# Optimization experiments

Hardware: AMD Instinct MI355X
Metric: run time of the kernel (lower is better)

Reference implementation:

```python
import jax, jax.numpy as jnp
import numpy as np

G = 8      # num_codebooks
D = 64     # codebook_dim
V = 1024   # codebook_size
BETA = 1.0


def setup_inputs() -> dict:
    key = jax.random.key(0)
    k1, k2, k3 = jax.random.split(key, 3)
    inputs = jax.random.normal(k1, (8, 2048, G * D), dtype=jnp.float32)
    paddings = jax.random.randint(k2, (8, 2048), 0, 2, dtype=jnp.int32)
    codebook = jax.random.normal(k3, (V, G, D), dtype=jnp.float32)
    return {"inputs": inputs, "paddings": paddings, "codebook": codebook}


def reference(inputs, paddings, codebook):
    B, T, _ = inputs.shape
    x = inputs.reshape(B, T, G, D)

    # Per-group L2 nearest neighbor: dist[b,t,g,v] = ||x - c||^2
    # ||x||^2 is constant over v, drop it for the argmin.
    dots = jnp.einsum("btgd,vgd->btgv", x, codebook)          # [B,T,G,V]
    c_sq = jnp.sum(codebook * codebook, axis=-1)                # [V,G]
    dists = c_sq.T[None, None] - 2.0 * dots                     # [B,T,G,V]
    ids = jnp.argmin(dists, axis=-1)                            # [B,T,G]

    # Gather selected codes per group.
    quantized = codebook[ids, jnp.arange(G)[None, None, :]]     # [B,T,G,D]

    mask = (1.0 - paddings.astype(jnp.float32))[:, :, None, None]  # [B,T,1,1]
    denom = mask.sum()
    xd = jax.lax.stop_gradient(x)
    qd = jax.lax.stop_gradient(quantized)
    kmeans_loss = jnp.sum((quantized - xd) ** 2 * mask) / denom
    commitment_loss = jnp.sum((x - qd) ** 2 * mask) / denom
    total_loss = kmeans_loss + BETA * commitment_loss

    # Straight-through estimator, masked.
    quantized_st = (x + jax.lax.stop_gradient(quantized - x)) * mask
    quantized_st = quantized_st.reshape(B, T, G * D)

    ids = jnp.where(mask[:, :, :, 0] == 0.0, -1, ids)           # [B,T,G]
    return ids, quantized_st, kmeans_loss, commitment_loss, total_loss
```

## Files before the change

### kernel.cpp

```cpp
#include <hip/hip_runtime.h>
#include <cfloat>
#include <stdint.h>

#define G_ 8
#define D_ 64
#define V_ 1024
#define BT_ 16384
#define TPB_ 512
#define PREPB_ 256
#define NSLOT_ 128
#define TOKS_ 128
#define NC_ 128
#define NCHUNK_ (V_ / NC_)

typedef unsigned long long u64;
typedef uint32_t u32;
typedef _Float16 h8 __attribute__((ext_vector_type(8)));
typedef _Float16 h4 __attribute__((ext_vector_type(4)));
typedef float f32x4 __attribute__((ext_vector_type(4)));

typedef __attribute__((address_space(3))) uint32_t lds_u32;
typedef __attribute__((address_space(1))) uint32_t glb_u32;

#define GL2LDS(gsrc, ldst) \
    __builtin_amdgcn_global_load_lds((glb_u32*)(gsrc), (lds_u32*)(ldst), 16, 0, 0)


__global__ void prep_csq(const float* __restrict__ cb, const int* __restrict__ pad,
                         float* __restrict__ csqT,
                         int* __restrict__ cnt, int* __restrict__ list,
                         float* __restrict__ out_ids, float* __restrict__ out_q,
                         _Float16* __restrict__ cbH, _Float16* __restrict__ cbL) {
    const int tid = threadIdx.x;
    const int idx = blockIdx.x * PREPB_ + tid;

    if (idx < V_ * G_) {
        const float4* r = (const float4*)(cb + (size_t)idx * D_);
        _Float16* hp = cbH + (size_t)idx * 64;
        _Float16* lp = cbL + (size_t)idx * 64;
        float s = 0.f;
#pragma unroll
        for (int i = 0; i < D_ / 4; ++i) {
            float4 c = r[i];
            s += c.x * c.x + c.y * c.y + c.z * c.z + c.w * c.w;
            float xs[4] = {c.x, c.y, c.z, c.w};
            h4 hv, lv;
#pragma unroll
            for (int e = 0; e < 4; ++e) {
                _Float16 hh = (_Float16)xs[e];
                hv[e] = hh;
                lv[e] = (_Float16)((xs[e] - (float)hh) * 4096.f);
            }
            *(h4*)(hp + i * 4) = hv;
            *(h4*)(lp + i * 4) = lv;
        }
        csqT[(idx & (G_ - 1)) * V_ + (idx >> 3)] = s;
    }

    __shared__ int s_cnt[8];
    __shared__ int s_base, s_npl;
    __shared__ int s_plist[PREPB_];
    const int lane = tid & 63, w = tid >> 6;
    const bool active = (pad[idx] == 0);
    u64 bal = __ballot(active);
    int na  = __popcll(bal);
    if (lane == 0) { s_cnt[w] = na; s_cnt[4 + w] = 64 - na; }
    __syncthreads();
    if (tid == 0) {
        int ta = s_cnt[0] + s_cnt[1] + s_cnt[2] + s_cnt[3];
        s_base = atomicAdd(cnt, ta);
        s_npl  = PREPB_ - ta;
    }
    __syncthreads();
    int pre_a = 0, pre_p = 0;
    for (int i = 0; i < w; ++i) { pre_a += s_cnt[i]; pre_p += s_cnt[4 + i]; }
    const u64 mb = ((u64)1 << lane) - 1;
    if (active) list[s_base + pre_a + __popcll(bal & mb)] = idx;
    else        s_plist[pre_p + __popcll(~bal & mb)] = idx;
    __syncthreads();

    const int npl = s_npl;
    for (int i = w; i < npl; i += 4) {
        int tok = s_plist[i];
        float4 z = make_float4(0.f, 0.f, 0.f, 0.f);
        float4* q = (float4*)(out_q + (size_t)tok * (G_ * D_)) + lane * 2;
        q[0] = z;
        q[1] = z;
        if (lane < G_) out_ids[(size_t)tok * G_ + lane] = -1.0f;
    }
}

__global__ __launch_bounds__(TPB_, 4) void vq_scan(
    const float* __restrict__ inp,
    const float* __restrict__ cb,
    const float* __restrict__ csqT,
    const int* __restrict__ cnt,
    const int* __restrict__ list,
    const _Float16* __restrict__ cbH,
    const _Float16* __restrict__ cbL,
    float* __restrict__ out_ids,
    float* __restrict__ out_q,
    float* __restrict__ part) {

    __shared__ __align__(16) unsigned char BH[2][NC_ * 128];
    __shared__ __align__(16) unsigned char BL[2][NC_ * 128];
    __shared__ float csq_s[V_];
    __shared__ u64 merge_s[2][TOKS_];

    const int nact = cnt[0];
    const int tile = blockIdx.x;
    if (tile * TOKS_ >= nact) return;
    const int g    = blockIdx.y;
    const int tid  = threadIdx.x;
    const int lane = tid & 63;
    const int w    = tid >> 6;
    const int mh   = w >> 1;
    const int nh   = w & 1;
    const int r16  = lane & 15;
    const int kq   = lane >> 4;

    const size_t soff = (size_t)(w * 8 + (lane >> 3)) * 1024
                      + (size_t)g * 128
                      + (size_t)(((lane & 7) ^ (lane >> 3)) * 16);
    const unsigned char* sH = (const unsigned char*)cbH + soff;
    const unsigned char* sL = (const unsigned char*)cbL + soff;
    const int ldsb = w * 1024;

    GL2LDS(sH,         &BH[0][ldsb]);
    GL2LDS(sH + 65536, &BH[0][ldsb + 8192]);
    GL2LDS(sL,         &BL[0][ldsb]);
    GL2LDS(sL + 65536, &BL[0][ldsb + 8192]);

    csq_s[tid]       = csqT[g * V_ + tid];
    csq_s[tid + 512] = csqT[g * V_ + tid + 512];

    h8 AH[2][2], AL[2][2];
#pragma unroll
    for (int rf = 0; rf < 2; ++rf) {
        int p = tile * TOKS_ + mh * 32 + rf * 16 + r16;
        int tok = list[p < nact ? p : 0];
        const float* xr = inp + (size_t)tok * (G_ * D_) + g * D_;
#pragma unroll
        for (int kf = 0; kf < 2; ++kf) {
            const float4* xp = (const float4*)(xr + kf * 32 + kq * 8);
            float4 a = xp[0], b = xp[1];
            float xs[8] = {a.x, a.y, a.z, a.w, b.x, b.y, b.z, b.w};
#pragma unroll
            for (int e = 0; e < 8; ++e) {
                _Float16 hh = (_Float16)xs[e];
                AH[rf][kf][e] = hh;
                AL[rf][kf][e] = (_Float16)((xs[e] - (float)hh) * 4096.f);
            }
        }
    }

    float beste[8];
    int   bestid[8];
#pragma unroll
    for (int s = 0; s < 8; ++s) { beste[s] = -FLT_MAX / 2; bestid[s] = 0; }

    __syncthreads();

    const u32 o0 = (u32)((((nh * 64 + r16) * 128 + kq * 16))
                         ^ ((u32)(r16 & 7) << 4));

    for (int c = 0; c < NCHUNK_; ++c) {
        const int cur = c & 1;
        const unsigned char* BHc = &BH[cur][0];
        const unsigned char* BLc = &BL[cur][0];

        if (c < NCHUNK_ - 1) {
            unsigned char* dH = &BH[cur ^ 1][ldsb];
            unsigned char* dL = &BL[cur ^ 1][ldsb];
            const unsigned char* nH = sH + (size_t)(c + 1) * 131072;
            const unsigned char* nL = sL + (size_t)(c + 1) * 131072;
            GL2LDS(nH,         dH);
            GL2LDS(nH + 65536, dH + 8192);
            GL2LDS(nL,         dL);
            GL2LDS(nL + 65536, dL + 8192);
        }

#pragma unroll 1
        for (int cf = 0; cf < 4; ++cf) {
            const u32 ob = o0 + (u32)(cf * 2048);
            const h8 bh0 = *(const h8*)(BHc + ob);
            const h8 bh1 = *(const h8*)(BHc + (ob ^ 64));
            const h8 bl0 = *(const h8*)(BLc + ob);
            const h8 bl1 = *(const h8*)(BLc + (ob ^ 64));
            const int vcol = c * NC_ + nh * 64 + cf * 16 + r16;
            const float ai = -0.5f * csq_s[vcol];
#pragma unroll
            for (int rf = 0; rf < 2; ++rf) {
                f32x4 a  = {ai, ai, ai, ai};
                f32x4 ac = {0.f, 0.f, 0.f, 0.f};
                a  = __builtin_amdgcn_mfma_f32_16x16x32_f16(AH[rf][0], bh0, a,  0, 0, 0);
                a  = __builtin_amdgcn_mfma_f32_16x16x32_f16(AH[rf][1], bh1, a,  0, 0, 0);
                ac = __builtin_amdgcn_mfma_f32_16x16x32_f16(AH[rf][0], bl0, ac, 0, 0, 0);
                ac = __builtin_amdgcn_mfma_f32_16x16x32_f16(AH[rf][1], bl1, ac, 0, 0, 0);
                ac = __builtin_amdgcn_mfma_f32_16x16x32_f16(AL[rf][0], bh0, ac, 0, 0, 0);
                ac = __builtin_amdgcn_mfma_f32_16x16x32_f16(AL[rf][1], bh1, ac, 0, 0, 0);
#pragma unroll
                for (int q = 0; q < 4; ++q) {
                    float e = fmaf(0x1.0p-12f, ac[q], a[q]);
                    int s = rf * 4 + q;
                    if (e > beste[s]) { beste[s] = e; bestid[s] = vcol; }
                }
            }
        }
        __syncthreads();
    }

#pragma unroll
    for (int s = 0; s < 8; ++s) {
        float d = -2.f * beste[s];
        u32 u = __float_as_uint(d);
        u = u ^ ((u >> 31) ? 0xFFFFFFFFu : 0x80000000u);
        u64 pk = ((u64)u << 32) | (u32)bestid[s];
#pragma unroll
        for (int off = 1; off <= 8; off <<= 1) {
            u64 o = __shfl_xor(pk, off, 64);
            pk = (o < pk) ? o : pk;
        }
        if (r16 == 0) {
            int row = mh * 32 + (s >> 2) * 16 + kq * 4 + (s & 3);
            merge_s[nh][row] = pk;
        }
    }
    __syncthreads();

    float l = 0.f;
    {
        int tl = tid >> 2, qv = tid & 3;
        int p  = tile * TOKS_ + tl;
        if (p < nact) {
            int tok = list[p];
            u64 qa = merge_s[0][tl], qb = merge_s[1][tl];
            u64 qm = (qb < qa) ? qb : qa;
            int id  = (int)(qm & 0xFFFFFFFFull);
            const float4* cr = (const float4*)(cb + ((size_t)id * G_ + g) * D_) + qv * 4;
            const float4* xr = (const float4*)(inp + (size_t)tok * (G_ * D_) + g * D_) + qv * 4;
            float4* qo = (float4*)(out_q + (size_t)tok * (G_ * D_) + g * D_) + qv * 4;
#pragma unroll
            for (int k = 0; k < 4; ++k) {
                float4 cc = cr[k], xx = xr[k];
                float dx = cc.x - xx.x, dy = cc.y - xx.y;
                float dz = cc.z - xx.z, dw = cc.w - xx.w;
                l += dx * dx + dy * dy + dz * dz + dw * dw;
                qo[k] = cc;
            }
            if (qv == 0) out_ids[(size_t)tok * G_ + g] = (float)id;
        }
    }
#pragma unroll
    for (int off = 32; off > 0; off >>= 1) l += __shfl_down(l, off, 64);
    if (lane == 0) {
        int slot = ((blockIdx.y * gridDim.x + blockIdx.x) * 8 + w) & (NSLOT_ - 1);
        atomicAdd(&part[slot], l);
    }
}

__global__ void finalize_kernel(const float* __restrict__ part,
                                const int* __restrict__ cnt,
                                float* __restrict__ out_losses) {
    int lane = threadIdx.x;
    float l = part[lane] + part[lane + 64];
#pragma unroll
    for (int off = 32; off > 0; off >>= 1) l += __shfl_down(l, off, 64);
    if (lane == 0) {
        float k = l / (float)cnt[0];
        out_losses[0] = k;
        out_losses[1] = k;
        out_losses[2] = 2.f * k;
    }
}

extern "C" void kernel_launch(void* const* d_in, const int* in_sizes, int n_in,
                              void* d_out, int out_size, void* d_ws, size_t ws_size,
                              hipStream_t stream) {
    const float* inp = (const float*)d_in[0];
    const int*   pad = (const int*)d_in[1];
    const float* cb  = (const float*)d_in[2];

    float* out   = (float*)d_out;
    float* o_ids = out;
    float* o_q   = out + (size_t)BT_ * G_;
    float* o_ls  = o_q + (size_t)BT_ * G_ * D_;

    float*     part = (float*)d_ws;
    int*       cnt  = (int*)((char*)d_ws + 512);
    float*     csqT = (float*)((char*)d_ws + 1024);
    int*       list = (int*)((char*)d_ws + 33792);
    _Float16*  cbH  = (_Float16*)((char*)d_ws + 131072);
    _Float16*  cbL  = (_Float16*)((char*)d_ws + 131072 + 1048576);

    hipMemsetAsync(d_ws, 0, 1024, stream);

    prep_csq<<<dim3(BT_ / PREPB_), dim3(PREPB_), 0, stream>>>(
        cb, pad, csqT, cnt, list, o_ids, o_q, cbH, cbL);

    dim3 grid(BT_ / TOKS_, G_);
    vq_scan<<<grid, dim3(TPB_), 0, stream>>>(
        inp, cb, csqT, cnt, list, cbH, cbL, o_ids, o_q, part);

    finalize_kernel<<<1, dim3(64), 0, stream>>>(part, cnt, o_ls);
}
```

Measured before the change: 138.7 us.

## Load codebook fragments directly from global memory and split V across waves

Removes the double-buffered LDS staging of the fp16 hi/lo codebook (global_load_lds plus per-chunk barriers). Each of four waves now scans its own quarter of the codebook for all 64 tokens of the tile, reading B fragments straight from global/L2, and the four partial argmins are merged in shared memory. Block size drops to 256 threads with 64 tokens per tile, and each wave holds four A row fragments. The point is to drop barrier and LDS overhead and raise A reuse per B load, at the price of more register pressure and uncoalesced, L2-dependent codebook reads.

After: 158.2 us. 14.1% more time.

```diff
diff --git a/kernel.cpp b/kernel.cpp
--- a/kernel.cpp
+++ b/kernel.cpp
@@ -6,24 +6,17 @@
 #define D_ 64
 #define V_ 1024
 #define BT_ 16384
-#define TPB_ 512
+#define TPB_ 256
 #define PREPB_ 256
 #define NSLOT_ 128
-#define TOKS_ 128
-#define NC_ 128
-#define NCHUNK_ (V_ / NC_)
+#define TOKS_ 64
+#define NCF_ 16
 
 typedef unsigned long long u64;
 typedef uint32_t u32;
 typedef _Float16 h8 __attribute__((ext_vector_type(8)));
 typedef _Float16 h4 __attribute__((ext_vector_type(4)));
 typedef float f32x4 __attribute__((ext_vector_type(4)));
-
-typedef __attribute__((address_space(3))) uint32_t lds_u32;
-typedef __attribute__((address_space(1))) uint32_t glb_u32;
-
-#define GL2LDS(gsrc, ldst) \
-    __builtin_amdgcn_global_load_lds((glb_u32*)(gsrc), (lds_u32*)(ldst), 16, 0, 0)
 
 
 __global__ void prep_csq(const float* __restrict__ cb, const int* __restrict__ pad,
@@ -90,7 +83,7 @@
     }
 }
 
-__global__ __launch_bounds__(TPB_, 4) void vq_scan(
+__global__ __launch_bounds__(TPB_, 3) void vq_scan(
     const float* __restrict__ inp,
     const float* __restrict__ cb,
     const float* __restrict__ csqT,
@@ -102,10 +95,7 @@
     float* __restrict__ out_q,
     float* __restrict__ part) {
 
-    __shared__ __align__(16) unsigned char BH[2][NC_ * 128];
-    __shared__ __align__(16) unsigned char BL[2][NC_ * 128];
-    __shared__ float csq_s[V_];
-    __shared__ u64 merge_s[2][TOKS_];
+    __shared__ u64 merge_s[4][TOKS_];
 
     const int nact = cnt[0];
     const int tile = blockIdx.x;
@@ -114,30 +104,13 @@
     const int tid  = threadIdx.x;
     const int lane = tid & 63;
     const int w    = tid >> 6;
-    const int mh   = w >> 1;
-    const int nh   = w & 1;
     const int r16  = lane & 15;
     const int kq   = lane >> 4;
 
-    const size_t soff = (size_t)(w * 8 + (lane >> 3)) * 1024
-                      + (size_t)g * 128
-                      + (size_t)(((lane & 7) ^ (lane >> 3)) * 16);
-    const unsigned char* sH = (const unsigned char*)cbH + soff;
-    const unsigned char* sL = (const unsigned char*)cbL + soff;
-    const int ldsb = w * 1024;
-
-    GL2LDS(sH,         &BH[0][ldsb]);
-    GL2LDS(sH + 65536, &BH[0][ldsb + 8192]);
-    GL2LDS(sL,         &BL[0][ldsb]);
-    GL2LDS(sL + 65536, &BL[0][ldsb + 8192]);
-
-    csq_s[tid]       = csqT[g * V_ + tid];
-    csq_s[tid + 512] = csqT[g * V_ + tid + 512];
-
-    h8 AH[2][2], AL[2][2];
-#pragma unroll
-    for (int rf = 0; rf < 2; ++rf) {
-        int p = tile * TOKS_ + mh * 32 + rf * 16 + r16;
+    h8 AH[4][2], AL[4][2];
+#pragma unroll
+    for (int rf = 0; rf < 4; ++rf) {
+        int p = tile * TOKS_ + rf * 16 + r16;
         int tok = list[p < nact ? p : 0];
         const float* xr = inp + (size_t)tok * (G_ * D_) + g * D_;
 #pragma unroll
@@ -154,64 +127,43 @@
         }
     }
 
-    float beste[8];
-    int   bestid[8];
-#pragma unroll
-    for (int s = 0; s < 8; ++s) { beste[s] = -FLT_MAX / 2; bestid[s] = 0; }
-
-    __syncthreads();
-
-    const u32 o0 = (u32)((((nh * 64 + r16) * 128 + kq * 16))
-                         ^ ((u32)(r16 & 7) << 4));
-
-    for (int c = 0; c < NCHUNK_; ++c) {
-        const int cur = c & 1;
-        const unsigned char* BHc = &BH[cur][0];
-        const unsigned char* BLc = &BL[cur][0];
-
-        if (c < NCHUNK_ - 1) {
-            unsigned char* dH = &BH[cur ^ 1][ldsb];
-            unsigned char* dL = &BL[cur ^ 1][ldsb];
-            const unsigned char* nH = sH + (size_t)(c + 1) * 131072;
-            const unsigned char* nL = sL + (size_t)(c + 1) * 131072;
-            GL2LDS(nH,         dH);
-            GL2LDS(nH + 65536, dH + 8192);
-            GL2LDS(nL,         dL);
-            GL2LDS(nL + 65536, dL + 8192);
-        }
-
-#pragma unroll 1
-        for (int cf = 0; cf < 4; ++cf) {
-            const u32 ob = o0 + (u32)(cf * 2048);
-            const h8 bh0 = *(const h8*)(BHc + ob);
-            const h8 bh1 = *(const h8*)(BHc + (ob ^ 64));
-            const h8 bl0 = *(const h8*)(BLc + ob);
-            const h8 bl1 = *(const h8*)(BLc + (ob ^ 64));
-            const int vcol = c * NC_ + nh * 64 + cf * 16 + r16;
-            const float ai = -0.5f * csq_s[vcol];
-#pragma unroll
-            for (int rf = 0; rf < 2; ++rf) {
-                f32x4 a  = {ai, ai, ai, ai};
-                f32x4 ac = {0.f, 0.f, 0.f, 0.f};
-                a  = __builtin_amdgcn_mfma_f32_16x16x32_f16(AH[rf][0], bh0, a,  0, 0, 0);
-                a  = __builtin_amdgcn_mfma_f32_16x16x32_f16(AH[rf][1], bh1, a,  0, 0, 0);
-                ac = __builtin_amdgcn_mfma_f32_16x16x32_f16(AH[rf][0], bl0, ac, 0, 0, 0);
-                ac = __builtin_amdgcn_mfma_f32_16x16x32_f16(AH[rf][1], bl1, ac, 0, 0, 0);
-                ac = __builtin_amdgcn_mfma_f32_16x16x32_f16(AL[rf][0], bh0, ac, 0, 0, 0);
-                ac = __builtin_amdgcn_mfma_f32_16x16x32_f16(AL[rf][1], bh1, ac, 0, 0, 0);
-#pragma unroll
-                for (int q = 0; q < 4; ++q) {
-                    float e = fmaf(0x1.0p-12f, ac[q], a[q]);
-                    int s = rf * 4 + q;
-                    if (e > beste[s]) { beste[s] = e; bestid[s] = vcol; }
-                }
-            }
-        }
-        __syncthreads();
-    }
-
-#pragma unroll
-    for (int s = 0; s < 8; ++s) {
+    float beste[16];
+    int   bestid[16];
+#pragma unroll
+    for (int s = 0; s < 16; ++s) { beste[s] = -FLT_MAX / 2; bestid[s] = 0; }
+
+    const int v0 = w * 256;
+#pragma unroll 2
+    for (int c = 0; c < NCF_; ++c) {
+        const int vc = v0 + c * 16 + r16;
+        const _Float16* bh = cbH + ((size_t)vc * G_ + g) * D_ + kq * 8;
+        const _Float16* bl = cbL + ((size_t)vc * G_ + g) * D_ + kq * 8;
+        const h8 bh0 = *(const h8*)bh;
+        const h8 bh1 = *(const h8*)(bh + 32);
+        const h8 bl0 = *(const h8*)bl;
+        const h8 bl1 = *(const h8*)(bl + 32);
+        const float ai = -0.5f * csqT[g * V_ + vc];
+#pragma unroll
+        for (int rf = 0; rf < 4; ++rf) {
+            f32x4 a  = {ai, ai, ai, ai};
+            f32x4 ac = {0.f, 0.f, 0.f, 0.f};
+            a  = __builtin_amdgcn_mfma_f32_16x16x32_f16(AH[rf][0], bh0, a,  0, 0, 0);
+            a  = __builtin_amdgcn_mfma_f32_16x16x32_f16(AH[rf][1], bh1, a,  0, 0, 0);
+            ac = __builtin_amdgcn_mfma_f32_16x16x32_f16(AH[rf][0], bl0, ac, 0, 0, 0);
+            ac = __builtin_amdgcn_mfma_f32_16x16x32_f16(AH[rf][1], bl1, ac, 0, 0, 0);
+            ac = __builtin_amdgcn_mfma_f32_16x16x32_f16(AL[rf][0], bh0, ac, 0, 0, 0);
+            ac = __builtin_amdgcn_mfma_f32_16x16x32_f16(AL[rf][1], bh1, ac, 0, 0, 0);
+#pragma unroll
+            for (int q = 0; q < 4; ++q) {
+                float e = fmaf(0x1.0p-12f, ac[q], a[q]);
+                int s = rf * 4 + q;
+                if (e > beste[s]) { beste[s] = e; bestid[s] = vc; }
+            }
+        }
+    }
+
+#pragma unroll
+    for (int s = 0; s < 16; ++s) {
         float d = -2.f * beste[s];
         u32 u = __float_as_uint(d);
         u = u ^ ((u >> 31) ? 0xFFFFFFFFu : 0x80000000u);
@@ -222,8 +174,8 @@
             pk = (o < pk) ? o : pk;
         }
         if (r16 == 0) {
-            int row = mh * 32 + (s >> 2) * 16 + kq * 4 + (s & 3);
-            merge_s[nh][row] = pk;
+            int row = (s >> 2) * 16 + kq * 4 + (s & 3);
+            merge_s[w][row] = pk;
         }
     }
     __syncthreads();
@@ -234,7 +186,10 @@
         int p  = tile * TOKS_ + tl;
         if (p < nact) {
             int tok = list[p];
-            u64 qa = merge_s[0][tl], qb = merge_s[1][tl];
+            u64 q0 = merge_s[0][tl], q1 = merge_s[1][tl];
+            u64 q2 = merge_s[2][tl], q3 = merge_s[3][tl];
+            u64 qa = (q1 < q0) ? q1 : q0;
+            u64 qb = (q3 < q2) ? q3 : q2;
             u64 qm = (qb < qa) ? qb : qa;
             int id  = (int)(qm & 0xFFFFFFFFull);
             const float4* cr = (const float4*)(cb + ((size_t)id * G_ + g) * D_) + qv * 4;
@@ -254,7 +209,7 @@
 #pragma unroll
     for (int off = 32; off > 0; off >>= 1) l += __shfl_down(l, off, 64);
     if (lane == 0) {
-        int slot = ((blockIdx.y * gridDim.x + blockIdx.x) * 8 + w) & (NSLOT_ - 1);
+        int slot = ((blockIdx.y * gridDim.x + blockIdx.x) * 4 + w) & (NSLOT_ - 1);
         atomicAdd(&part[slot], l);
     }
 }
```

## Halve block size, deepen codebook LDS pipeline to 4 buffers with raw barriers

Applied to the files above, without the earlier changes.

The scan kernel now runs with 256 threads per block, each wave owning 64 tokens instead of 32. Codebook chunks shrink to 64 codes and go through a 4-deep LDS ring with three chunks prefetched ahead. Each iteration uses one manual vmcnt wait plus s_barrier in place of __syncthreads after compute. The goal is more B-fragment reuse per LDS read and better hiding of global-to-LDS latency. In exchange it doubles per-thread accumulator and A-fragment registers, lowers the occupancy target, and relies on hand-counted vmcnt values being correct.

After: 134.6 us. 1.03x faster.

```diff
diff --git a/kernel.cpp b/kernel.cpp
--- a/kernel.cpp
+++ b/kernel.cpp
@@ -6,11 +6,12 @@
 #define D_ 64
 #define V_ 1024
 #define BT_ 16384
-#define TPB_ 512
+#define TPB_ 256
 #define PREPB_ 256
 #define NSLOT_ 128
 #define TOKS_ 128
-#define NC_ 128
+#define NC_ 64
+#define NB_ 4
 #define NCHUNK_ (V_ / NC_)
 
 typedef unsigned long long u64;
@@ -90,7 +91,7 @@
     }
 }
 
-__global__ __launch_bounds__(TPB_, 4) void vq_scan(
+__global__ __launch_bounds__(TPB_, 2) void vq_scan(
     const float* __restrict__ inp,
     const float* __restrict__ cb,
     const float* __restrict__ csqT,
@@ -102,8 +103,8 @@
     float* __restrict__ out_q,
     float* __restrict__ part) {
 
-    __shared__ __align__(16) unsigned char BH[2][NC_ * 128];
-    __shared__ __align__(16) unsigned char BL[2][NC_ * 128];
+    __shared__ __align__(16) unsigned char BH[NB_][NC_ * 128];
+    __shared__ __align__(16) unsigned char BL[NB_][NC_ * 128];
     __shared__ float csq_s[V_];
     __shared__ u64 merge_s[2][TOKS_];
 
@@ -119,25 +120,10 @@
     const int r16  = lane & 15;
     const int kq   = lane >> 4;
 
-    const size_t soff = (size_t)(w * 8 + (lane >> 3)) * 1024
-                      + (size_t)g * 128
-                      + (size_t)(((lane & 7) ^ (lane >> 3)) * 16);
-    const unsigned char* sH = (const unsigned char*)cbH + soff;
-    const unsigned char* sL = (const unsigned char*)cbL + soff;
-    const int ldsb = w * 1024;
-
-    GL2LDS(sH,         &BH[0][ldsb]);
-    GL2LDS(sH + 65536, &BH[0][ldsb + 8192]);
-    GL2LDS(sL,         &BL[0][ldsb]);
-    GL2LDS(sL + 65536, &BL[0][ldsb + 8192]);
-
-    csq_s[tid]       = csqT[g * V_ + tid];
-    csq_s[tid + 512] = csqT[g * V_ + tid + 512];
-
-    h8 AH[2][2], AL[2][2];
-#pragma unroll
-    for (int rf = 0; rf < 2; ++rf) {
-        int p = tile * TOKS_ + mh * 32 + rf * 16 + r16;
+    h8 AH[4][2], AL[4][2];
+#pragma unroll
+    for (int rf = 0; rf < 4; ++rf) {
+        int p = tile * TOKS_ + mh * 64 + rf * 16 + r16;
         int tok = list[p < nact ? p : 0];
         const float* xr = inp + (size_t)tok * (G_ * D_) + g * D_;
 #pragma unroll
@@ -154,43 +140,69 @@
         }
     }
 
-    float beste[8];
-    int   bestid[8];
-#pragma unroll
-    for (int s = 0; s < 8; ++s) { beste[s] = -FLT_MAX / 2; bestid[s] = 0; }
-
-    __syncthreads();
-
-    const u32 o0 = (u32)((((nh * 64 + r16) * 128 + kq * 16))
+    const size_t soff = (size_t)(w * 16 + (lane >> 3)) * 1024
+                      + (size_t)g * 128
+                      + (size_t)(((lane & 7) ^ (lane >> 3)) * 16);
+    const unsigned char* sH = (const unsigned char*)cbH + soff;
+    const unsigned char* sL = (const unsigned char*)cbL + soff;
+    const int ldsb = w * 2048;
+
+#pragma unroll
+    for (int c0 = 0; c0 < 3; ++c0) {
+        const size_t adv = (size_t)c0 * 65536;
+        GL2LDS(sH + adv,        &BH[c0][ldsb]);
+        GL2LDS(sH + adv + 8192, &BH[c0][ldsb + 1024]);
+        GL2LDS(sL + adv,        &BL[c0][ldsb]);
+        GL2LDS(sL + adv + 8192, &BL[c0][ldsb + 1024]);
+    }
+
+    csq_s[tid]       = csqT[g * V_ + tid];
+    csq_s[tid + 256] = csqT[g * V_ + tid + 256];
+    csq_s[tid + 512] = csqT[g * V_ + tid + 512];
+    csq_s[tid + 768] = csqT[g * V_ + tid + 768];
+
+    float beste[16];
+    int   bestid[16];
+#pragma unroll
+    for (int s = 0; s < 16; ++s) { beste[s] = -FLT_MAX / 2; bestid[s] = 0; }
+
+    asm volatile("s_waitcnt lgkmcnt(0)" ::: "memory");
+
+    const u32 o0 = (u32)((((nh * 32 + r16) * 128 + kq * 16))
                          ^ ((u32)(r16 & 7) << 4));
 
+#pragma unroll 1
     for (int c = 0; c < NCHUNK_; ++c) {
-        const int cur = c & 1;
-        const unsigned char* BHc = &BH[cur][0];
-        const unsigned char* BLc = &BL[cur][0];
-
-        if (c < NCHUNK_ - 1) {
-            unsigned char* dH = &BH[cur ^ 1][ldsb];
-            unsigned char* dL = &BL[cur ^ 1][ldsb];
-            const unsigned char* nH = sH + (size_t)(c + 1) * 131072;
-            const unsigned char* nL = sL + (size_t)(c + 1) * 131072;
-            GL2LDS(nH,         dH);
-            GL2LDS(nH + 65536, dH + 8192);
-            GL2LDS(nL,         dL);
-            GL2LDS(nL + 65536, dL + 8192);
-        }
-
-#pragma unroll 1
-        for (int cf = 0; cf < 4; ++cf) {
+        if (c < NCHUNK_ - 2)
+            asm volatile("s_waitcnt vmcnt(8)\n\ts_barrier" ::: "memory");
+        else if (c == NCHUNK_ - 2)
+            asm volatile("s_waitcnt vmcnt(4)\n\ts_barrier" ::: "memory");
+        else
+            asm volatile("s_waitcnt vmcnt(0)\n\ts_barrier" ::: "memory");
+        __builtin_amdgcn_sched_barrier(0);
+
+        if (c + 3 < NCHUNK_) {
+            const int b = (c + 3) & (NB_ - 1);
+            const size_t adv = (size_t)(c + 3) * 65536;
+            GL2LDS(sH + adv,        &BH[b][ldsb]);
+            GL2LDS(sH + adv + 8192, &BH[b][ldsb + 1024]);
+            GL2LDS(sL + adv,        &BL[b][ldsb]);
+            GL2LDS(sL + adv + 8192, &BL[b][ldsb + 1024]);
+        }
+
+        const unsigned char* BHc = &BH[c & (NB_ - 1)][0];
+        const unsigned char* BLc = &BL[c & (NB_ - 1)][0];
+#pragma unroll
+        for (int cf = 0; cf < 2; ++cf) {
             const u32 ob = o0 + (u32)(cf * 2048);
             const h8 bh0 = *(const h8*)(BHc + ob);
             const h8 bh1 = *(const h8*)(BHc + (ob ^ 64));
             const h8 bl0 = *(const h8*)(BLc + ob);
             const h8 bl1 = *(const h8*)(BLc + (ob ^ 64));
-            const int vcol = c * NC_ + nh * 64 + cf * 16 + r16;
+            const int vcol = c * NC_ + nh * 32 + cf * 16 + r16;
             const float ai = -0.5f * csq_s[vcol];
 #pragma unroll
-            for (int rf = 0; rf < 2; ++rf) {
+            for (int rf = 0; rf < 4; ++rf) {
                 f32x4 a  = {ai, ai, ai, ai};
                 f32x4 ac = {0.f, 0.f, 0.f, 0.f};
                 a  = __builtin_amdgcn_mfma_f32_16x16x32_f16(AH[rf][0], bh0, a,  0, 0, 0);
@@ -207,11 +219,10 @@
                 }
             }
         }
-        __syncthreads();
-    }
-
-#pragma unroll
-    for (int s = 0; s < 8; ++s) {
+    }
+
+#pragma unroll
+    for (int s = 0; s < 16; ++s) {
         float d = -2.f * beste[s];
         u32 u = __float_as_uint(d);
         u = u ^ ((u >> 31) ? 0xFFFFFFFFu : 0x80000000u);
@@ -222,7 +233,7 @@
             pk = (o < pk) ? o : pk;
         }
         if (r16 == 0) {
-            int row = mh * 32 + (s >> 2) * 16 + kq * 4 + (s & 3);
+            int row = mh * 64 + (s >> 2) * 16 + kq * 4 + (s & 3);
             merge_s[nh][row] = pk;
         }
     }
@@ -230,18 +241,18 @@
 
     float l = 0.f;
     {
-        int tl = tid >> 2, qv = tid & 3;
+        int tl = tid >> 1, qv = tid & 1;
         int p  = tile * TOKS_ + tl;
         if (p < nact) {
             int tok = list[p];
             u64 qa = merge_s[0][tl], qb = merge_s[1][tl];
             u64 qm = (qb < qa) ? qb : qa;
             int id  = (int)(qm & 0xFFFFFFFFull);
-            const float4* cr = (const float4*)(cb + ((size_t)id * G_ + g) * D_) + qv * 4;
-            const float4* xr = (const float4*)(inp + (size_t)tok * (G_ * D_) + g * D_) + qv * 4;
-            float4* qo = (float4*)(out_q + (size_t)tok * (G_ * D_) + g * D_) + qv * 4;
-#pragma unroll
-            for (int k = 0; k < 4; ++k) {
+            const float4* cr = (const float4*)(cb + ((size_t)id * G_ + g) * D_) + qv * 8;
+            const float4* xr = (const float4*)(inp + (size_t)tok * (G_ * D_) + g * D_) + qv * 8;
+            float4* qo = (float4*)(out_q + (size_t)tok * (G_ * D_) + g * D_) + qv * 8;
+#pragma unroll
+            for (int k = 0; k < 8; ++k) {
                 float4 cc = cr[k], xx = xr[k];
                 float dx = cc.x - xx.x, dy = cc.y - xx.y;
                 float dz = cc.z - xx.z, dw = cc.w - xx.w;
@@ -254,7 +265,7 @@
 #pragma unroll
     for (int off = 32; off > 0; off >>= 1) l += __shfl_down(l, off, 64);
     if (lane == 0) {
-        int slot = ((blockIdx.y * gridDim.x + blockIdx.x) * 8 + w) & (NSLOT_ - 1);
+        int slot = ((blockIdx.y * gridDim.x + blockIdx.x) * 4 + w) & (NSLOT_ - 1);
         atomicAdd(&part[slot], l);
     }
 }
```

## Halve block and chunk size, restructure codebook double-buffer with single barrier

Applied to the files above, without the earlier changes.

Block size drops from 512 to 256 threads, with 64 tokens per tile and 64-code chunks, so there are more, smaller blocks and less LDS per block. Codebook prefetch now starts after the A fragments are built. The main loop is restructured to one vmcnt wait plus barrier at the top of each chunk, which replaces the trailing __syncthreads, and the inner loop is fully unrolled. The intent is better occupancy and latency hiding, at the cost of more chunk iterations, more barriers overall and more repeated codebook loads across tiles.

Result: no change. 137.7 us (-0.7%).

```diff
diff --git a/kernel.cpp b/kernel.cpp
--- a/kernel.cpp
+++ b/kernel.cpp
@@ -6,11 +6,12 @@
 #define D_ 64
 #define V_ 1024
 #define BT_ 16384
-#define TPB_ 512
+#define TPB_ 256
 #define PREPB_ 256
 #define NSLOT_ 128
-#define TOKS_ 128
-#define NC_ 128
+#define TOKS_ 64
+#define NC_ 64
+#define NB_ 2
 #define NCHUNK_ (V_ / NC_)
 
 typedef unsigned long long u64;
@@ -102,8 +103,8 @@
     float* __restrict__ out_q,
     float* __restrict__ part) {
 
-    __shared__ __align__(16) unsigned char BH[2][NC_ * 128];
-    __shared__ __align__(16) unsigned char BL[2][NC_ * 128];
+    __shared__ __align__(16) unsigned char BH[NB_][NC_ * 128];
+    __shared__ __align__(16) unsigned char BL[NB_][NC_ * 128];
     __shared__ float csq_s[V_];
     __shared__ u64 merge_s[2][TOKS_];
 
@@ -119,21 +120,6 @@
     const int r16  = lane & 15;
     const int kq   = lane >> 4;
 
-    const size_t soff = (size_t)(w * 8 + (lane >> 3)) * 1024
-                      + (size_t)g * 128
-                      + (size_t)(((lane & 7) ^ (lane >> 3)) * 16);
-    const unsigned char* sH = (const unsigned char*)cbH + soff;
-    const unsigned char* sL = (const unsigned char*)cbL + soff;
-    const int ldsb = w * 1024;
-
-    GL2LDS(sH,         &BH[0][ldsb]);
-    GL2LDS(sH + 65536, &BH[0][ldsb + 8192]);
-    GL2LDS(sL,         &BL[0][ldsb]);
-    GL2LDS(sL + 65536, &BL[0][ldsb + 8192]);
-
-    csq_s[tid]       = csqT[g * V_ + tid];
-    csq_s[tid + 512] = csqT[g * V_ + tid + 512];
-
     h8 AH[2][2], AL[2][2];
 #pragma unroll
     for (int rf = 0; rf < 2; ++rf) {
@@ -154,40 +140,57 @@
         }
     }
 
+    const size_t soff = (size_t)(w * 16 + (lane >> 3)) * 1024
+                      + (size_t)g * 128
+                      + (size_t)(((lane & 7) ^ (lane >> 3)) * 16);
+    const unsigned char* sH = (const unsigned char*)cbH + soff;
+    const unsigned char* sL = (const unsigned char*)cbL + soff;
+    const int ldsb = w * 2048;
+
+    GL2LDS(sH,        &BH[0][ldsb]);
+    GL2LDS(sH + 8192, &BH[0][ldsb + 1024]);
+    GL2LDS(sL,        &BL[0][ldsb]);
+    GL2LDS(sL + 8192, &BL[0][ldsb + 1024]);
+
+    csq_s[tid]       = csqT[g * V_ + tid];
+    csq_s[tid + 256] = csqT[g * V_ + tid + 256];
+    csq_s[tid + 512] = csqT[g * V_ + tid + 512];
+    csq_s[tid + 768] = csqT[g * V_ + tid + 768];
+
     float beste[8];
     int   bestid[8];
 #pragma unroll
     for (int s = 0; s < 8; ++s) { beste[s] = -FLT_MAX / 2; bestid[s] = 0; }
 
-    __syncthreads();
-
-    const u32 o0 = (u32)((((nh * 64 + r16) * 128 + kq * 16))
+    asm volatile("s_waitcnt lgkmcnt(0)" ::: "memory");
+
+    const u32 o0 = (u32)((((nh * 32 + r16) * 128 + kq * 16))
                          ^ ((u32)(r16 & 7) << 4));
 
+#pragma unroll 1
     for (int c = 0; c < NCHUNK_; ++c) {
-        const int cur = c & 1;
-        const unsigned char* BHc = &BH[cur][0];
-        const unsigned char* BLc = &BL[cur][0];
-
-        if (c < NCHUNK_ - 1) {
-            unsigned char* dH = &BH[cur ^ 1][ldsb];
-            unsigned char* dL = &BL[cur ^ 1][ldsb];
-            const unsigned char* nH = sH + (size_t)(c + 1) * 131072;
-            const unsigned char* nL = sL + (size_t)(c + 1) * 131072;
-            GL2LDS(nH,         dH);
-            GL2LDS(nH + 65536, dH + 8192);
-            GL2LDS(nL,         dL);
-            GL2LDS(nL + 65536, dL + 8192);
-        }
-
-#pragma unroll 1
-        for (int cf = 0; cf < 4; ++cf) {
+        asm volatile("s_waitcnt vmcnt(0)\n\ts_barrier" ::: "memory");
+        __builtin_amdgcn_sched_barrier(0);
+
+        if (c + 1 < NCHUNK_) {
+            const int b = (c + 1) & 1;
+            const size_t adv = (size_t)(c + 1) * 65536;
+            GL2LDS(sH + adv,        &BH[b][ldsb]);
+            GL2LDS(sH + adv + 8192, &BH[b][ldsb + 1024]);
+            GL2LDS(sL + adv,        &BL[b][ldsb]);
+            GL2LDS(sL + adv + 8192, &BL[b][ldsb + 1024]);
+        }
+
+        const unsigned char* BHc = &BH[c & 1][0];
+        const unsigned char* BLc = &BL[c & 1][0];
+#pragma unroll
+        for (int cf = 0; cf < 2; ++cf) {
             const u32 ob = o0 + (u32)(cf * 2048);
             const h8 bh0 = *(const h8*)(BHc + ob);
             const h8 bh1 = *(const h8*)(BHc + (ob ^ 64));
             const h8 bl0 = *(const h8*)(BLc + ob);
             const h8 bl1 = *(const h8*)(BLc + (ob ^ 64));
-            const int vcol = c * NC_ + nh * 64 + cf * 16 + r16;
+            const int vcol = c * NC_ + nh * 32 + cf * 16 + r16;
             const float ai = -0.5f * csq_s[vcol];
 #pragma unroll
             for (int rf = 0; rf < 2; ++rf) {
@@ -207,7 +210,6 @@
                 }
             }
         }
-        __syncthreads();
     }
 
 #pragma unroll
@@ -254,7 +256,7 @@
 #pragma unroll
     for (int off = 32; off > 0; off >>= 1) l += __shfl_down(l, off, 64);
     if (lane == 0) {
-        int slot = ((blockIdx.y * gridDim.x + blockIdx.x) * 8 + w) & (NSLOT_ - 1);
+        int slot = ((blockIdx.y * gridDim.x + blockIdx.x) * 4 + w) & (NSLOT_ - 1);
         atomicAdd(&part[slot], l);
     }
 }
```
